# Kernel optimization log

Measured on AMD Instinct MI355X. Metric: run time of the kernel, lower is better.

Reference implementation:

```python
import jax, jax.numpy as jnp
import numpy as np

DEPTH = 3  # chemprop default message passing depth


def setup_inputs() -> dict:
    key = jax.random.key(0)
    ks = jax.random.split(key, 10)
    n_atoms, n_bonds, max_nb, n_mols = 50000, 100000, 6, 2000
    atom_fdim, bond_fdim, hidden = 133, 147, 300
    f_atoms = jax.random.normal(ks[0], (n_atoms, atom_fdim), dtype=jnp.float32)
    f_bonds = jax.random.normal(ks[1], (n_bonds, bond_fdim), dtype=jnp.float32)
    a2b = jax.random.randint(ks[2], (n_atoms, max_nb), 0, n_bonds, dtype=jnp.int32)
    b2a = jax.random.randint(ks[3], (n_bonds,), 0, n_atoms, dtype=jnp.int32)
    b2revb = jax.random.randint(ks[4], (n_bonds,), 0, n_bonds, dtype=jnp.int32)
    mol_id = jnp.sort(jax.random.randint(ks[5], (n_atoms,), 0, n_mols, dtype=jnp.int32))
    W_i = jax.random.normal(ks[6], (bond_fdim, hidden), dtype=jnp.float32) * 0.05
    W_h = jax.random.normal(ks[7], (hidden, hidden), dtype=jnp.float32) * 0.05
    W_o = jax.random.normal(ks[8], (atom_fdim + hidden, hidden), dtype=jnp.float32) * 0.05
    b_o = jnp.zeros((hidden,), dtype=jnp.float32)
    return {"f_atoms": f_atoms, "f_bonds": f_bonds, "a2b": a2b, "b2a": b2a,
            "b2revb": b2revb, "mol_id": mol_id, "n_mols": n_mols,
            "W_i": W_i, "W_h": W_h, "W_o": W_o, "b_o": b_o}


def reference(f_atoms, f_bonds, a2b, b2a, b2revb, mol_id, n_mols, W_i, W_h, W_o, b_o):
    act = jax.nn.relu
    # W_i: bond features -> hidden; message init
    inp = f_bonds @ W_i                      # [n_bonds, h]
    message = act(inp)
    for _ in range(DEPTH - 1):
        nei = message[a2b]                    # [n_atoms, max_nb, h] gather
        a_message = nei.sum(axis=1)           # [n_atoms, h]
        rev = message[b2revb]                 # [n_bonds, h]
        message = a_message[b2a] - rev        # [n_bonds, h]
        message = act(inp + message @ W_h)
    # final atom readout
    a_message = message[a2b].sum(axis=1)      # [n_atoms, h]
    a_input = jnp.concatenate([f_atoms, a_message], axis=1)  # [n_atoms, fa+h]
    atom_hiddens = act(a_input @ W_o + b_o)   # [n_atoms, h]
    # ragged per-molecule mean (a_scope loop -> segment mean)
    sums = jax.ops.segment_sum(atom_hiddens, mol_id, num_segments=n_mols)
    counts = jax.ops.segment_sum(jnp.ones((atom_hiddens.shape[0],), dtype=atom_hiddens.dtype), mol_id, num_segments=n_mols)
    mol_vecs = jnp.where(counts[:, None] > 0, sums / jnp.maximum(counts, 1.0)[:, None], 0.0)
    return mol_vecs
```

## Files before the change

### kernel.cpp

```cpp
#include <hip/hip_runtime.h>
#include <cstddef>

#define H 300
#define RS 304
#define MAXNB 6
#define ASTR 312

typedef __attribute__((ext_vector_type(8)))  short bf16x8;
typedef __attribute__((ext_vector_type(16))) float f32x16;

__device__ __forceinline__ float bf2f(unsigned short u) {
    return __uint_as_float(((unsigned int)u) << 16);
}
__device__ __forceinline__ unsigned short f2bf(float f) {
    unsigned int u = __float_as_uint(f);
    u += 0x7FFFu + ((u >> 16) & 1u);
    return (unsigned short)(u >> 16);
}
__device__ __forceinline__ unsigned int sub2bf(unsigned int a, unsigned int b) {
    float d0 = bf2f((unsigned short)(a & 0xFFFFu)) - bf2f((unsigned short)(b & 0xFFFFu));
    float d1 = bf2f((unsigned short)(a >> 16))     - bf2f((unsigned short)(b >> 16));
    return (unsigned int)f2bf(d0) | ((unsigned int)f2bf(d1) << 16);
}
__device__ __forceinline__ unsigned int relu2(unsigned int w) {
    unsigned int r = w;
    if (w & 0x80000000u) r &= 0x0000FFFFu;
    if (w & 0x00008000u) r &= 0xFFFF0000u;
    return r;
}
__device__ __forceinline__ uint4 relu4(uint4 v) {
    v.x = relu2(v.x); v.y = relu2(v.y); v.z = relu2(v.z); v.w = relu2(v.w);
    return v;
}
__device__ __forceinline__ uint4 subpack4(uint4 a, uint4 b) {
    uint4 r;
    r.x = sub2bf(a.x, b.x); r.y = sub2bf(a.y, b.y);
    r.z = sub2bf(a.z, b.z); r.w = sub2bf(a.w, b.w);
    return r;
}


__global__ void __launch_bounds__(256)
pack_a_f32(const float* __restrict__ src, unsigned short* __restrict__ dst,
           int M, int K, int S, int MB)
{
    int g = blockIdx.x * 256 + threadIdx.x;
    int total = MB * S * 32;
    if (g >= total) return;
    int mrow = g & 31;
    int t = g >> 5;
    int s = t % S;
    int m_blk = t / S;
    int m = m_blk * 32 + mrow;
    unsigned int w[8];
#pragma unroll
    for (int q = 0; q < 2; ++q) {
#pragma unroll
        for (int p = 0; p < 4; ++p) {
            int k = s * 16 + q * 8 + p * 2;
            unsigned short h0 = (m < M && k     < K) ? f2bf(src[(size_t)m * K + k])     : (unsigned short)0;
            unsigned short h1 = (m < M && k + 1 < K) ? f2bf(src[(size_t)m * K + k + 1]) : (unsigned short)0;
            w[q * 4 + p] = (unsigned int)h0 | ((unsigned int)h1 << 16);
        }
    }
    size_t base = ((size_t)(m_blk * S + s) * 64) * 8;
    *(uint4*)&dst[base + (size_t)(0 * 32 + mrow) * 8] = make_uint4(w[0], w[1], w[2], w[3]);
    *(uint4*)&dst[base + (size_t)(1 * 32 + mrow) * 8] = make_uint4(w[4], w[5], w[6], w[7]);
}

__global__ void __launch_bounds__(256)
pack_b(const float* __restrict__ src1, const float* __restrict__ src2,
       unsigned short* __restrict__ dst, int K1, int S1, int K2, int SB)
{
    int g = blockIdx.x * 256 + threadIdx.x;
    if (g >= 10 * SB * 64) return;
    int lane = g & 63;
    int t = g >> 6;
    int s = t % SB;
    int n_blk = t / SB;
    int n = n_blk * 32 + (lane & 31);
    unsigned int w[4];
#pragma unroll
    for (int p = 0; p < 4; ++p) {
        unsigned short h[2];
#pragma unroll
        for (int e = 0; e < 2; ++e) {
            int kf = s * 16 + (lane >> 5) * 8 + p * 2 + e;
            float v = 0.0f;
            if (n < H) {
                if (s < S1) {
                    if (kf < K1) v = src1[(size_t)kf * H + n];
                } else {
                    int k2 = kf - S1 * 16;
                    if (k2 < K2) v = src2[(size_t)k2 * H + n];
                }
            }
            h[e] = f2bf(v);
        }
        w[p] = (unsigned int)h[0] | ((unsigned int)h[1] << 16);
    }
    *(uint4*)&dst[(size_t)g * 8] = make_uint4(w[0], w[1], w[2], w[3]);
}

template<int RELU>
__global__ void __launch_bounds__(256)
aggregate_row(const unsigned short* __restrict__ msg, const int* __restrict__ a2b,
              unsigned short* __restrict__ amsg, int n_atoms)
{
    int gid = blockIdx.x * 256 + threadIdx.x;
    int total = n_atoms * 38;
    if (gid >= total) return;
    int atom = gid / 38;
    int g8 = gid - atom * 38;
    const int* nb = a2b + atom * MAXNB;
    float sum[8] = {};
#pragma unroll
    for (int j = 0; j < MAXNB; ++j) {
        int b = nb[j];
        uint4 v = *(const uint4*)&msg[(size_t)b * RS + g8 * 8];
        if (RELU) v = relu4(v);
        unsigned int ww[4] = {v.x, v.y, v.z, v.w};
#pragma unroll
        for (int p = 0; p < 4; ++p) {
            sum[p * 2]     += bf2f((unsigned short)(ww[p] & 0xFFFFu));
            sum[p * 2 + 1] += bf2f((unsigned short)(ww[p] >> 16));
        }
    }
    unsigned int ow[4];
#pragma unroll
    for (int p = 0; p < 4; ++p)
        ow[p] = (unsigned int)f2bf(sum[p * 2]) | ((unsigned int)f2bf(sum[p * 2 + 1]) << 16);
    *(uint4*)&amsg[(size_t)atom * RS + g8 * 8] = make_uint4(ow[0], ow[1], ow[2], ow[3]);
}

template<int S1, int S2, int SBL, int MODE, int RELUMSG>
__global__ void __launch_bounds__(256)
gemm_fused(const unsigned short* __restrict__ A1,
           const unsigned short* __restrict__ amsg,
           const unsigned short* __restrict__ msg,
           const int* __restrict__ b2a, const int* __restrict__ b2revb,
           const unsigned short* __restrict__ Bp,
           const float* __restrict__ bias,
           const unsigned short* __restrict__ inp_add,
           unsigned short* __restrict__ out, int M)
{
    __shared__ __align__(16) unsigned short smem[64 * ASTR];

    const int lane  = threadIdx.x & 63;
    const int w     = threadIdx.x >> 6;
    const int rbase = (w >> 1) * 32;
    const int cbase = (w & 1) * 160;
    const int mrow  = lane & 31;
    const int quad  = lane >> 5;
    const int m0    = blockIdx.x * 64;
    const int m_blk = blockIdx.x * 2 + (w >> 1);
    const int nblk0 = cbase >> 5;

    if (MODE == 1 || MODE == 2) {
        const int r = threadIdx.x >> 2;
        const int q = threadIdx.x & 3;
        int mm = m0 + r;
        int mv = (mm < M) ? mm : 0;
        const unsigned short* rowA;
        const unsigned short* rowM = nullptr;
        if (MODE == 1) {
            rowA = amsg + (size_t)b2a[mv] * RS;
            rowM = msg  + (size_t)b2revb[mv] * RS;
        } else {
            rowA = amsg + (size_t)mv * RS;
        }
#pragma unroll
        for (int i = 0; i < 10; ++i) {
            int c = q + i * 4;
            if (c < 38) {
                uint4 o;
                if (MODE == 1) {
                    uint4 va = *(const uint4*)(rowA + c * 8);
                    uint4 vm = *(const uint4*)(rowM + c * 8);
                    if (RELUMSG) vm = relu4(vm);
                    o = subpack4(va, vm);
                } else {
                    o = *(const uint4*)(rowA + c * 8);
                }
                *(uint4*)&smem[r * ASTR + c * 8] = o;
            }
        }
        __syncthreads();
    }

    f32x16 acc[5];
#pragma unroll
    for (int t = 0; t < 5; ++t)
#pragma unroll
        for (int i = 0; i < 16; ++i) acc[t][i] = 0.0f;

    const unsigned short* pa1 = (S1 > 0) ? (A1 + ((size_t)m_blk * S1 * 64 + lane) * 8) : nullptr;
    const unsigned short* pb  = Bp + ((size_t)nblk0 * SBL * 64 + lane) * 8;

    constexpr int STOT = S1 + S2;

    auto loadA = [&](int s) -> bf16x8 {
        if (s < S1) return *(const bf16x8*)(pa1 + (size_t)s * 512);
        return *(const bf16x8*)&smem[(rbase + mrow) * ASTR + (s - S1) * 16 + quad * 8];
    };

    bf16x8 b0[5], b1[5];
#pragma unroll
    for (int nt = 0; nt < 5; ++nt) b0[nt] = *(const bf16x8*)(pb + ((size_t)nt * SBL + 0) * 512);
    if (STOT > 1) {
#pragma unroll
        for (int nt = 0; nt < 5; ++nt) b1[nt] = *(const bf16x8*)(pb + ((size_t)nt * SBL + 1) * 512);
    }

#pragma unroll
    for (int s = 0; s < STOT; s += 2) {
        bf16x8 a = loadA(s);
        acc[0] = __builtin_amdgcn_mfma_f32_32x32x16_bf16(a, b0[0], acc[0], 0, 0, 0);
        acc[1] = __builtin_amdgcn_mfma_f32_32x32x16_bf16(a, b0[1], acc[1], 0, 0, 0);
        acc[2] = __builtin_amdgcn_mfma_f32_32x32x16_bf16(a, b0[2], acc[2], 0, 0, 0);
        acc[3] = __builtin_amdgcn_mfma_f32_32x32x16_bf16(a, b0[3], acc[3], 0, 0, 0);
        acc[4] = __builtin_amdgcn_mfma_f32_32x32x16_bf16(a, b0[4], acc[4], 0, 0, 0);
        if (s + 2 < STOT) {
#pragma unroll
            for (int nt = 0; nt < 5; ++nt) b0[nt] = *(const bf16x8*)(pb + ((size_t)nt * SBL + s + 2) * 512);
        }
        if (s + 1 < STOT) {
            bf16x8 a2 = loadA(s + 1);
            acc[0] = __builtin_amdgcn_mfma_f32_32x32x16_bf16(a2, b1[0], acc[0], 0, 0, 0);
            acc[1] = __builtin_amdgcn_mfma_f32_32x32x16_bf16(a2, b1[1], acc[1], 0, 0, 0);
            acc[2] = __builtin_amdgcn_mfma_f32_32x32x16_bf16(a2, b1[2], acc[2], 0, 0, 0);
            acc[3] = __builtin_amdgcn_mfma_f32_32x32x16_bf16(a2, b1[3], acc[3], 0, 0, 0);
            acc[4] = __builtin_amdgcn_mfma_f32_32x32x16_bf16(a2, b1[4], acc[4], 0, 0, 0);
            if (s + 3 < STOT) {
#pragma unroll
                for (int nt = 0; nt < 5; ++nt) b1[nt] = *(const bf16x8*)(pb + ((size_t)nt * SBL + s + 3) * 512);
            }
        }
    }

    __syncthreads();

#pragma unroll
    for (int nt = 0; nt < 5; ++nt) {
        int col = cbase + nt * 32 + mrow;
#pragma unroll
        for (int r = 0; r < 16; ++r) {
            int row = rbase + (r & 3) + 8 * (r >> 2) + 4 * quad;
            if (col < 308) smem[row * 308 + col] = f2bf(acc[nt][r]);
        }
    }
    __syncthreads();

    for (int idx = threadIdx.x; idx < 64 * 76; idx += 256) {
        int row = idx / 76, gcol = idx - row * 76;
        int mm = m0 + row;
        if (mm >= M) continue;
        int c0 = gcol * 4;
        uint2 raw = *(const uint2*)&smem[row * 308 + c0];
        uint2 o;
        if (MODE == 0) {
            o = raw;
        } else {
            unsigned short h[4] = {(unsigned short)(raw.x & 0xFFFFu), (unsigned short)(raw.x >> 16),
                                   (unsigned short)(raw.y & 0xFFFFu), (unsigned short)(raw.y >> 16)};
            float v[4];
#pragma unroll
            for (int e = 0; e < 4; ++e) v[e] = bf2f(h[e]);
            if (MODE == 1) {
                uint2 iv = *(const uint2*)&inp_add[(size_t)mm * RS + c0];
                v[0] += bf2f((unsigned short)(iv.x & 0xFFFFu));
                v[1] += bf2f((unsigned short)(iv.x >> 16));
                v[2] += bf2f((unsigned short)(iv.y & 0xFFFFu));
                v[3] += bf2f((unsigned short)(iv.y >> 16));
            } else {
#pragma unroll
                for (int e = 0; e < 4; ++e) v[e] += (c0 + e < H) ? bias[c0 + e] : 0.0f;
            }
#pragma unroll
            for (int e = 0; e < 4; ++e) h[e] = f2bf(fmaxf(v[e], 0.0f));
            o.x = (unsigned int)h[0] | ((unsigned int)h[1] << 16);
            o.y = (unsigned int)h[2] | ((unsigned int)h[3] << 16);
        }
        *(uint2*)&out[(size_t)mm * RS + c0] = o;
    }
}

__global__ void __launch_bounds__(128)
segmean_kernel(const unsigned short* __restrict__ ah,
               const int* __restrict__ mol_id, int n_atoms,
               float* __restrict__ out)
{
    int m = blockIdx.x;
    int lo = 0, hi = n_atoms;
    while (lo < hi) { int mid = (lo + hi) >> 1; if (mol_id[mid] < m) lo = mid + 1; else hi = mid; }
    int start = lo;
    hi = n_atoms;
    while (lo < hi) { int mid = (lo + hi) >> 1; if (mol_id[mid] < m + 1) lo = mid + 1; else hi = mid; }
    int end = lo;

    int c = threadIdx.x;
    float a0 = 0.f, a1 = 0.f, a2 = 0.f;
    for (int a = start; a < end; ++a) {
        const unsigned short* row = ah + (size_t)a * RS;
        a0 += bf2f(row[c]);
        a1 += bf2f(row[c + 128]);
        if (c < H - 256) a2 += bf2f(row[c + 256]);
    }
    float inv = (end > start) ? 1.0f / (float)(end - start) : 0.0f;
    float* orow = out + (size_t)m * H;
    orow[c] = a0 * inv;
    orow[c + 128] = a1 * inv;
    if (c < H - 256) orow[c + 256] = a2 * inv;
}

extern "C" void kernel_launch(void* const* d_in, const int* in_sizes, int n_in,
                              void* d_out, int out_size, void* d_ws, size_t ws_size,
                              hipStream_t stream)
{
    const float* f_atoms = (const float*)d_in[0];
    const float* f_bonds = (const float*)d_in[1];
    const int*   a2b     = (const int*)d_in[2];
    const int*   b2a     = (const int*)d_in[3];
    const int*   b2revb  = (const int*)d_in[4];
    const int*   mol_id  = (const int*)d_in[5];
    const float* W_i     = (const float*)d_in[7];
    const float* W_h     = (const float*)d_in[8];
    const float* W_o     = (const float*)d_in[9];
    const float* b_o     = (const float*)d_in[10];

    const int n_atoms   = in_sizes[5];
    const int n_bonds   = in_sizes[3];
    const int atom_fdim = in_sizes[0] / n_atoms;
    const int bond_fdim = in_sizes[1] / n_bonds;
    const int n_mols    = out_size / H;

    const int gBonds = (n_bonds + 63) / 64;
    const int gAtoms = (n_atoms + 63) / 64;
    const int MBb = 2 * gBonds;
    const int MBa = 2 * gAtoms;

    const size_t bondsRS = (size_t)n_bonds * RS;
    const size_t atomsRS = (size_t)n_atoms * RS;
    const size_t fbpSz   = (size_t)MBb * 10 * 512;
    const size_t wihSz   = 10 * 30 * 512;
    const size_t woSz    = 10 * 29 * 512;
    const size_t wh19Sz  = 10 * 19 * 512;

    unsigned short* inp  = (unsigned short*)d_ws;
    unsigned short* msgB = inp  + bondsRS;
    unsigned short* amsg = msgB + bondsRS;
    unsigned short* fbp  = amsg + atomsRS;
    unsigned short* wih  = fbp  + fbpSz;
    unsigned short* wo   = wih  + wihSz;
    unsigned short* wh19 = wo   + woSz;
    unsigned short* fap  = inp;
    unsigned short* ah   = fbp;

    dim3 blk(256);
    const int aggBlocks = (n_atoms * 38 + 255) / 256;

    pack_b<<<(10 * 30 * 64 + 255) / 256, blk, 0, stream>>>(W_i, W_h, wih, bond_fdim, 10, H, 30);
    pack_b<<<(10 * 19 * 64 + 255) / 256, blk, 0, stream>>>(W_h, W_h, wh19, H, 19, 0, 19);
    pack_b<<<(10 * 29 * 64 + 255) / 256, blk, 0, stream>>>(W_o, W_o + (size_t)atom_fdim * H, wo,
                                                           atom_fdim, 9, H, 29);
    pack_a_f32<<<(MBb * 10 * 32 + 255) / 256, blk, 0, stream>>>(f_bonds, fbp, n_bonds, bond_fdim, 10, MBb);

    gemm_fused<10, 0, 30, 0, 0><<<gBonds, blk, 0, stream>>>(
        fbp, nullptr, nullptr, nullptr, nullptr, wih, nullptr, nullptr, inp, n_bonds);

    aggregate_row<1><<<aggBlocks, blk, 0, stream>>>(inp, a2b, amsg, n_atoms);
    gemm_fused<0, 19, 19, 1, 1><<<gBonds, blk, 0, stream>>>(
        nullptr, amsg, inp, b2a, b2revb, wh19, nullptr, inp, msgB, n_bonds);

    aggregate_row<0><<<aggBlocks, blk, 0, stream>>>(msgB, a2b, amsg, n_atoms);
    gemm_fused<0, 19, 19, 1, 0><<<gBonds, blk, 0, stream>>>(
        nullptr, amsg, msgB, b2a, b2revb, wh19, nullptr, inp, inp, n_bonds);

    aggregate_row<0><<<aggBlocks, blk, 0, stream>>>(inp, a2b, amsg, n_atoms);

    pack_a_f32<<<(MBa * 9 * 32 + 255) / 256, blk, 0, stream>>>(f_atoms, fap, n_atoms, atom_fdim, 9, MBa);

    gemm_fused<9, 19, 29, 2, 0><<<gAtoms, blk, 0, stream>>>(
        fap, amsg, nullptr, nullptr, nullptr, wo, b_o, nullptr, ah, n_atoms);

    segmean_kernel<<<n_mols, dim3(128), 0, stream>>>(ah, mol_id, n_atoms, (float*)d_out);
}
```

Baseline: 543.2 us.

## Fuse f_bonds bf16 conversion into first GEMM and stage atom packing via LDS

The first GEMM now reads f32 bond features directly, converts them to bf16 and stages them in shared memory, so the separate pack kernel and its intermediate buffer are gone. The atom-feature pack kernel is rewritten to read rows coalesced into LDS, then write the MFMA-blocked layout. Together these cut a kernel launch and a full write and read of the packed bond buffer. The fused path costs an extra LDS staging step and a __syncthreads in the GEMM.

```diff
diff --git a/kernel.cpp b/kernel.cpp
--- a/kernel.cpp
+++ b/kernel.cpp
@@ -40,32 +40,43 @@
 }
 
 
+template<int S>
 __global__ void __launch_bounds__(256)
-pack_a_f32(const float* __restrict__ src, unsigned short* __restrict__ dst,
-           int M, int K, int S, int MB)
-{
-    int g = blockIdx.x * 256 + threadIdx.x;
-    int total = MB * S * 32;
-    if (g >= total) return;
-    int mrow = g & 31;
-    int t = g >> 5;
-    int s = t % S;
-    int m_blk = t / S;
-    int m = m_blk * 32 + mrow;
-    unsigned int w[8];
-#pragma unroll
-    for (int q = 0; q < 2; ++q) {
-#pragma unroll
-        for (int p = 0; p < 4; ++p) {
-            int k = s * 16 + q * 8 + p * 2;
-            unsigned short h0 = (m < M && k     < K) ? f2bf(src[(size_t)m * K + k])     : (unsigned short)0;
-            unsigned short h1 = (m < M && k + 1 < K) ? f2bf(src[(size_t)m * K + k + 1]) : (unsigned short)0;
-            w[q * 4 + p] = (unsigned int)h0 | ((unsigned int)h1 << 16);
-        }
-    }
-    size_t base = ((size_t)(m_blk * S + s) * 64) * 8;
-    *(uint4*)&dst[base + (size_t)(0 * 32 + mrow) * 8] = make_uint4(w[0], w[1], w[2], w[3]);
-    *(uint4*)&dst[base + (size_t)(1 * 32 + mrow) * 8] = make_uint4(w[4], w[5], w[6], w[7]);
+pack_a_f32_c(const float* __restrict__ src, unsigned short* __restrict__ dst,
+             int M, int K)
+{
+    __shared__ unsigned short sm[64 * 152];
+    const int m0 = blockIdx.x * 64;
+    const int r = threadIdx.x >> 2;
+    const int q = threadIdx.x & 3;
+    int mv = m0 + r; if (mv >= M) mv = M - 1;
+    const float* rowF = src + (size_t)mv * K;
+#pragma unroll
+    for (int i = 0; i < (S * 4 + 3) / 4; ++i) {
+        int c = q + i * 4;
+        if (c * 4 < S * 16) {
+            unsigned short h[4];
+#pragma unroll
+            for (int e = 0; e < 4; ++e) {
+                int k = c * 4 + e;
+                h[e] = (k < K) ? f2bf(rowF[k]) : (unsigned short)0;
+            }
+            uint2 o;
+            o.x = (unsigned int)h[0] | ((unsigned int)h[1] << 16);
+            o.y = (unsigned int)h[2] | ((unsigned int)h[3] << 16);
+            *(uint2*)&sm[r * 152 + c * 4] = o;
+        }
+    }
+    __syncthreads();
+    for (int j = threadIdx.x; j < 2 * S * 64; j += 256) {
+        int lane = j & 63;
+        int t = j >> 6;
+        int s = t % S;
+        int mb2 = t / S;
+        uint4 v = *(const uint4*)&sm[(mb2 * 32 + (lane & 31)) * 152 + s * 16 + (lane >> 5) * 8];
+        int m_blk = blockIdx.x * 2 + mb2;
+        *(uint4*)&dst[((size_t)(m_blk * S + s) * 64 + lane) * 8] = v;
+    }
 }
 
 __global__ void __launch_bounds__(256)
@@ -142,6 +153,7 @@
            const unsigned short* __restrict__ Bp,
            const float* __restrict__ bias,
            const unsigned short* __restrict__ inp_add,
+           const float* __restrict__ Adense, int Kd,
            unsigned short* __restrict__ out, int M)
 {
     __shared__ __align__(16) unsigned short smem[64 * ASTR];
@@ -156,36 +168,58 @@
     const int m_blk = blockIdx.x * 2 + (w >> 1);
     const int nblk0 = cbase >> 5;
 
-    if (MODE == 1 || MODE == 2) {
+    {
         const int r = threadIdx.x >> 2;
         const int q = threadIdx.x & 3;
         int mm = m0 + r;
         int mv = (mm < M) ? mm : 0;
-        const unsigned short* rowA;
-        const unsigned short* rowM = nullptr;
-        if (MODE == 1) {
-            rowA = amsg + (size_t)b2a[mv] * RS;
-            rowM = msg  + (size_t)b2revb[mv] * RS;
-        } else {
-            rowA = amsg + (size_t)mv * RS;
-        }
-#pragma unroll
-        for (int i = 0; i < 10; ++i) {
-            int c = q + i * 4;
-            if (c < 38) {
-                uint4 o;
-                if (MODE == 1) {
-                    uint4 va = *(const uint4*)(rowA + c * 8);
-                    uint4 vm = *(const uint4*)(rowM + c * 8);
-                    if (RELUMSG) vm = relu4(vm);
-                    o = subpack4(va, vm);
-                } else {
-                    o = *(const uint4*)(rowA + c * 8);
+        if (MODE == 0) {
+            if (mm >= M) mv = M - 1;
+            const float* rowF = Adense + (size_t)mv * Kd;
+#pragma unroll
+            for (int i = 0; i < (S2 * 4 + 3) / 4; ++i) {
+                int c = q + i * 4;
+                if (c * 4 < S2 * 16) {
+                    unsigned short h[4];
+#pragma unroll
+                    for (int e = 0; e < 4; ++e) {
+                        int k = c * 4 + e;
+                        h[e] = (k < Kd) ? f2bf(rowF[k]) : (unsigned short)0;
+                    }
+                    uint2 o;
+                    o.x = (unsigned int)h[0] | ((unsigned int)h[1] << 16);
+                    o.y = (unsigned int)h[2] | ((unsigned int)h[3] << 16);
+                    *(uint2*)&smem[r * ASTR + c * 4] = o;
                 }
-                *(uint4*)&smem[r * ASTR + c * 8] = o;
-            }
-        }
-        __syncthreads();
+            }
+            __syncthreads();
+        } else if (MODE == 1 || MODE == 2) {
+            const unsigned short* rowA;
+            const unsigned short* rowM = nullptr;
+            if (MODE == 1) {
+                rowA = amsg + (size_t)b2a[mv] * RS;
+                rowM = msg  + (size_t)b2revb[mv] * RS;
+            } else {
+                rowA = amsg + (size_t)mv * RS;
+            }
+#pragma unroll
+            for (int i = 0; i < 10; ++i) {
+                int c = q + i * 4;
+                if (c < 38) {
+                    uint4 o;
+                    if (MODE == 1) {
+                        uint4 va = *(const uint4*)(rowA + c * 8);
+                        uint4 vm = *(const uint4*)(rowM + c * 8);
+                        if (RELUMSG) vm = relu4(vm);
+                        o = subpack4(va, vm);
+                    } else {
+                        o = *(const uint4*)(rowA + c * 8);
+                    }
+                    *(uint4*)&smem[r * ASTR + c * 8] = o;
+                }
+            }
+            __syncthreads();
+        }
     }
 
     f32x16 acc[5];
@@ -336,12 +370,11 @@
 
     const int gBonds = (n_bonds + 63) / 64;
     const int gAtoms = (n_atoms + 63) / 64;
-    const int MBb = 2 * gBonds;
     const int MBa = 2 * gAtoms;
 
     const size_t bondsRS = (size_t)n_bonds * RS;
     const size_t atomsRS = (size_t)n_atoms * RS;
-    const size_t fbpSz   = (size_t)MBb * 10 * 512;
+    const size_t fapSz   = (size_t)MBa * 9 * 512;
     const size_t wihSz   = 10 * 30 * 512;
     const size_t woSz    = 10 * 29 * 512;
     const size_t wh19Sz  = 10 * 19 * 512;
@@ -349,12 +382,11 @@
     unsigned short* inp  = (unsigned short*)d_ws;
     unsigned short* msgB = inp  + bondsRS;
     unsigned short* amsg = msgB + bondsRS;
-    unsigned short* fbp  = amsg + atomsRS;
-    unsigned short* wih  = fbp  + fbpSz;
+    unsigned short* wih  = amsg + atomsRS;
     unsigned short* wo   = wih  + wihSz;
     unsigned short* wh19 = wo   + woSz;
+    unsigned short* ah   = wh19 + wh19Sz;
     unsigned short* fap  = inp;
-    unsigned short* ah   = fbp;
 
     dim3 blk(256);
     const int aggBlocks = (n_atoms * 38 + 255) / 256;
@@ -363,25 +395,25 @@
     pack_b<<<(10 * 19 * 64 + 255) / 256, blk, 0, stream>>>(W_h, W_h, wh19, H, 19, 0, 19);
     pack_b<<<(10 * 29 * 64 + 255) / 256, blk, 0, stream>>>(W_o, W_o + (size_t)atom_fdim * H, wo,
                                                            atom_fdim, 9, H, 29);
-    pack_a_f32<<<(MBb * 10 * 32 + 255) / 256, blk, 0, stream>>>(f_bonds, fbp, n_bonds, bond_fdim, 10, MBb);
-
-    gemm_fused<10, 0, 30, 0, 0><<<gBonds, blk, 0, stream>>>(
-        fbp, nullptr, nullptr, nullptr, nullptr, wih, nullptr, nullptr, inp, n_bonds);
+
+    gemm_fused<0, 10, 30, 0, 0><<<gBonds, blk, 0, stream>>>(
+        nullptr, nullptr, nullptr, nullptr, nullptr, wih, nullptr, nullptr,
+        f_bonds, bond_fdim, inp, n_bonds);
 
     aggregate_row<1><<<aggBlocks, blk, 0, stream>>>(inp, a2b, amsg, n_atoms);
     gemm_fused<0, 19, 19, 1, 1><<<gBonds, blk, 0, stream>>>(
-        nullptr, amsg, inp, b2a, b2revb, wh19, nullptr, inp, msgB, n_bonds);
+        nullptr, amsg, inp, b2a, b2revb, wh19, nullptr, inp, nullptr, 0, msgB, n_bonds);
 
     aggregate_row<0><<<aggBlocks, blk, 0, stream>>>(msgB, a2b, amsg, n_atoms);
     gemm_fused<0, 19, 19, 1, 0><<<gBonds, blk, 0, stream>>>(
-        nullptr, amsg, msgB, b2a, b2revb, wh19, nullptr, inp, inp, n_bonds);
+        nullptr, amsg, msgB, b2a, b2revb, wh19, nullptr, inp, nullptr, 0, inp, n_bonds);
 
     aggregate_row<0><<<aggBlocks, blk, 0, stream>>>(inp, a2b, amsg, n_atoms);
 
-    pack_a_f32<<<(MBa * 9 * 32 + 255) / 256, blk, 0, stream>>>(f_atoms, fap, n_atoms, atom_fdim, 9, MBa);
+    pack_a_f32_c<9><<<gAtoms, blk, 0, stream>>>(f_atoms, fap, n_atoms, atom_fdim);
 
     gemm_fused<9, 19, 29, 2, 0><<<gAtoms, blk, 0, stream>>>(
-        fap, amsg, nullptr, nullptr, nullptr, wo, b_o, nullptr, ah, n_atoms);
+        fap, amsg, nullptr, nullptr, nullptr, wo, b_o, nullptr, nullptr, 0, ah, n_atoms);
 
     segmean_kernel<<<n_mols, dim3(128), 0, stream>>>(ah, mol_id, n_atoms, (float*)d_out);
 }
```

Result: faster. 516.6 us (-4.9%).
